# Optimization experiments

Measured on AMD Instinct MI355X. Metric: run time of the kernel, lower is better.

The kernel has to match this reference:

```python
import jax, jax.numpy as jnp
import numpy as np

B, C, T = 128, 19, 1000

def _conv2d(x, w, pad, groups=1):
    return jax.lax.conv_general_dilated(x, w, (1, 1), [(pad[0], pad[0]), (pad[1], pad[1])],
                                        dimension_numbers=('NCHW', 'OIHW', 'NCHW'),
                                        feature_group_count=groups)

def _conv1d(x, w, pad):
    return jax.lax.conv_general_dilated(x, w, (1,), [(pad, pad)],
                                        dimension_numbers=('NCH', 'OIH', 'NCH'))

def _bn(x, g, b, axis=1):
    # eval-mode BatchNorm with running_mean=0, running_var=1 -> pure affine
    shp = [1] * x.ndim
    shp[axis] = -1
    return x * g.reshape(shp) + b.reshape(shp)

def _gat(x, W, a_src, a_dst, bias, src, dst, ew):
    # GATConv, concat=False (head mean); messages scaled by external edge weight ew
    N = x.shape[0]
    H, D = a_src.shape
    h = (x @ W).reshape(N, H, D)
    e = jax.nn.leaky_relu((h * a_src).sum(-1)[src] + (h * a_dst).sum(-1)[dst], 0.2)  # [E,H]
    emax = jax.ops.segment_max(e, dst, num_segments=N)
    ee = jnp.exp(e - emax[dst])
    alpha = ee / (jax.ops.segment_sum(ee, dst, num_segments=N)[dst] + 1e-16)
    msg = (alpha * ew[:, None])[:, :, None] * h[src]  # [E,H,D]
    return jax.ops.segment_sum(msg, dst, num_segments=N).mean(1) + bias

def setup_inputs():
    key = jax.random.key(0)
    ks = iter(jax.random.split(key, 48))
    def nrm(shape, s=0.1):
        return jax.random.normal(next(ks), shape, jnp.float32) * s
    ii = np.arange(C)
    base = np.arange(B)[:, None] * C
    src = (base + np.repeat(ii, C)[None, :]).reshape(-1)
    dst = (base + np.tile(ii, C)[None, :]).reshape(-1)
    return {
        'x': nrm((B, C, T), 1.0),
        'conv1_w': nrm((16, 1, 1, 25)),
        'bn1_g': 1.0 + nrm((16,)), 'bn1_b': nrm((16,)),
        'depth_w': nrm((16, 1, C, 1)),
        'bn2_g': 1.0 + nrm((16,)), 'bn2_b': nrm((16,)),
        'se_w1': nrm((16, 4)), 'se_w2': nrm((4, 16)),
        'sep_w': nrm((16, 16, 1, 16)),
        'bn3_g': 1.0 + nrm((16,)), 'bn3_b': nrm((16,)),
        'ms_w0': nrm((16, 1, 15)), 'ms_g0': 1.0 + nrm((16,)), 'ms_b0': nrm((16,)),
        'ms_w1': nrm((16, 1, 25)), 'ms_g1': 1.0 + nrm((16,)), 'ms_b1': nrm((16,)),
        'ms_w2': nrm((16, 1, 35)), 'ms_g2': 1.0 + nrm((16,)), 'ms_b2': nrm((16,)),
        'adj_w': nrm((32, 1)), 'adj_b': nrm((1,)),
        'gat1_w': nrm((32, 8 * 64), 0.05), 'gat1_as': nrm((8, 64)), 'gat1_ad': nrm((8, 64)), 'gat1_bias': nrm((64,)),
        'skip1_w': nrm((32, 64)), 'skip1_b': nrm((64,)),
        'bng1_g': 1.0 + nrm((64,)), 'bng1_b': nrm((64,)),
        'gat2_w': nrm((64, 8 * 64), 0.05), 'gat2_as': nrm((8, 64)), 'gat2_ad': nrm((8, 64)), 'gat2_bias': nrm((64,)),
        'bng2_g': 1.0 + nrm((64,)), 'bng2_b': nrm((64,)),
        'cls_w1': nrm((64, 64)), 'cls_b1': nrm((64,)),
        'cls_w2': nrm((64, 2)), 'cls_b2': nrm((2,)),
        'edge_index': jnp.asarray(np.stack([src, dst]), dtype=jnp.int32),
        'batch_idx': jnp.repeat(jnp.arange(B, dtype=jnp.int32), C),
    }

def reference(x, conv1_w, bn1_g, bn1_b, depth_w, bn2_g, bn2_b, se_w1, se_w2, sep_w, bn3_g, bn3_b,
              ms_w0, ms_g0, ms_b0, ms_w1, ms_g1, ms_b1, ms_w2, ms_g2, ms_b2,
              adj_w, adj_b, gat1_w, gat1_as, gat1_ad, gat1_bias, skip1_w, skip1_b, bng1_g, bng1_b,
              gat2_w, gat2_as, gat2_ad, gat2_bias, bng2_g, bng2_b, cls_w1, cls_b1, cls_w2, cls_b2,
              edge_index, batch_idx):
    Bn, Cn, Tn = x.shape
    gelu = lambda v: jax.nn.gelu(v, approximate=False)
    # --- EEGNet-style frontend ---
    y = _conv2d(x[:, None], conv1_w, (0, 12))                 # [B,16,C,T]
    y = _bn(y, bn1_g, bn1_b)
    y = _conv2d(y, depth_w, (0, 0), groups=16)                # depthwise over channels -> [B,16,1,T]
    y = jax.nn.elu(_bn(y, bn2_g, bn2_b))
    s = y.mean((2, 3))                                        # SE squeeze [B,16]
    s = jax.nn.sigmoid(gelu(s @ se_w1) @ se_w2)
    y = y * s[:, :, None, None]
    y = y.reshape(Bn, 16, 1, Tn // 4, 4).mean(-1)             # AvgPool2d((1,4))
    y = jax.nn.elu(_bn(_conv2d(y, sep_w, (0, 8)), bn3_g, bn3_b))
    yv = y.mean((2, 3))                                       # AdaptiveAvgPool2d((C,1)): 1->C replicates
    y_nodes = jnp.broadcast_to(yv[:, None, :], (Bn, Cn, 16)).reshape(Bn * Cn, 16)
    # --- per-channel multiscale conv1d ---
    z = x.reshape(Bn * Cn, 1, Tn)
    acc = jax.nn.elu(_bn(_conv1d(z, ms_w0, 7), ms_g0, ms_b0))
    acc = acc + jax.nn.elu(_bn(_conv1d(z, ms_w1, 12), ms_g1, ms_b1))
    acc = acc + jax.nn.elu(_bn(_conv1d(z, ms_w2, 17), ms_g2, ms_b2))
    z = (acc / 3.0).mean(-1)                                  # AdaptiveAvgPool1d(1) -> [N,16]
    feat = jnp.concatenate([y_nodes, z], axis=1)              # [N,32]
    # --- edge-weighted GAT stack ---
    scores = jax.nn.sigmoid(feat @ adj_w + adj_b).reshape(-1)
    src, dst = edge_index[0], edge_index[1]
    ew = scores[src] * scores[dst]
    h = _gat(feat, gat1_w, gat1_as, gat1_ad, gat1_bias, src, dst, ew)
    h = gelu(_bn(h, bng1_g, bng1_b) + feat @ skip1_w + skip1_b)
    h2 = _gat(h, gat2_w, gat2_as, gat2_ad, gat2_bias, src, dst, ew)
    h = gelu(_bn(h2, bng2_g, bng2_b) + h2)
    # --- global mean pool + classifier ---
    gs = jax.ops.segment_sum(h, batch_idx, num_segments=Bn)
    cnt = jax.ops.segment_sum(jnp.ones((Bn * Cn, 1), h.dtype), batch_idx, num_segments=Bn)
    g = gs / cnt
    return gelu(g @ cls_w1 + cls_b1) @ cls_w2 + cls_b2
```

## Files before the change

kernel.cpp:

```cpp
#include <hip/hip_runtime.h>
#include <hip/hip_bf16.h>
#include <math.h>

#define BATCH 128
#define NCH 19
#define TLEN 1000
#define NNODES (BATCH * NCH)

__device__ __forceinline__ float eluf(float x) { return x > 0.f ? x : expm1f(x); }
__device__ __forceinline__ float geluf(float x) { return 0.5f * x * (1.f + erff(x * 0.70710678118654752f)); }
__device__ __forceinline__ float sigf(float x) { return 1.f / (1.f + expf(-x)); }
__device__ __forceinline__ float lrelu(float x) { return x > 0.f ? x : 0.2f * x; }

__global__ __launch_bounds__(256) void k_pool(
    const float* __restrict__ x, const float* __restrict__ w1,
    const float* __restrict__ bn1g, const float* __restrict__ bn1b,
    const float* __restrict__ dw, const float* __restrict__ bn2g,
    const float* __restrict__ bn2b, float* __restrict__ y4g,
    float* __restrict__ ssum) {
  int blk = blockIdx.x;
  int b = blk >> 4, f = blk & 15;
  int tid = threadIdx.x;
  __shared__ float xw[1024];
  __shared__ float dws[19], w1s[25];
  __shared__ float redw[4];
  if (tid < 19) dws[tid] = dw[f * 19 + tid];
  else if (tid >= 32 && tid < 57) w1s[tid - 32] = w1[f * 25 + tid - 32];
  __syncthreads();
  const float* xb = x + (size_t)b * NCH * TLEN;
  for (int i = tid; i < 1024; i += 256) {
    int t = i - 12;
    float v = 0.f;
    if (t >= 0 && t < TLEN) {
#pragma unroll
      for (int c = 0; c < 19; c++) v += dws[c] * xb[c * TLEN + t];
    }
    xw[i] = v;
  }
  __syncthreads();
  float g1 = bn1g[f], b1 = bn1b[f];
  float g2 = bn2g[f], b2 = bn2b[f];
  float sumdw = 0.f;
#pragma unroll
  for (int c = 0; c < 19; c++) sumdw += dws[c];
  float scale = g2 * g1, cb = g2 * b1 * sumdw + b2;
  float part = 0.f;
  if (tid < 250) {
    float pool = 0.f;
#pragma unroll
    for (int q = 0; q < 4; q++) {
      int t = 4 * tid + q;
      float acc = 0.f;
#pragma unroll
      for (int k = 0; k < 25; k++) acc += w1s[k] * xw[t + k];
      pool += eluf(scale * acc + cb);
    }
    part = pool;
    y4g[(size_t)(b * 16 + f) * 250 + tid] = pool * 0.25f;
  }
  int lane = tid & 63, wid = tid >> 6;
  for (int off = 32; off > 0; off >>= 1) part += __shfl_down(part, off, 64);
  if (lane == 0) redw[wid] = part;
  __syncthreads();
  if (tid == 0) ssum[b * 16 + f] = redw[0] + redw[1] + redw[2] + redw[3];
}

__global__ __launch_bounds__(256) void k_sep(
    const float* __restrict__ y4g, const float* __restrict__ ssum,
    const float* __restrict__ sew1, const float* __restrict__ sew2,
    const float* __restrict__ sw, const float* __restrict__ g3,
    const float* __restrict__ b3, float* __restrict__ yv) {
  int blk = blockIdx.x;
  int b = blk >> 4, fo = blk & 15;
  int tid = threadIdx.x;
  __shared__ float yloc[16 * 268];
  __shared__ float sws[256];
  __shared__ float s_s[16], se_s[16], u4[4];
  __shared__ float redw[4];
  sws[tid] = sw[fo * 256 + tid];
  if (tid < 16) s_s[tid] = ssum[b * 16 + tid] * (1.f / 1000.f);
  __syncthreads();
  if (tid < 4) {
    float a = 0.f;
#pragma unroll
    for (int ff = 0; ff < 16; ff++) a += s_s[ff] * sew1[ff * 4 + tid];
    u4[tid] = geluf(a);
  }
  __syncthreads();
  if (tid < 16) {
    float a = 0.f;
#pragma unroll
    for (int j = 0; j < 4; j++) a += u4[j] * sew2[j * 16 + tid];
    se_s[tid] = sigf(a);
  }
  __syncthreads();
#pragma unroll
  for (int fi = 0; fi < 16; fi++) {
    float sc = se_s[fi];
    const float* yr = y4g + (size_t)(b * 16 + fi) * 250;
    for (int j = tid; j < 268; j += 256) {
      float v = (j >= 8 && j < 258) ? yr[j - 8] * sc : 0.f;
      yloc[fi * 268 + j] = v;
    }
  }
  __syncthreads();
  float accsum = 0.f;
  if (tid < 251) {
    float acc = 0.f;
#pragma unroll
    for (int fi = 0; fi < 16; fi++) {
      const float* yr = &yloc[fi * 268 + tid];
      const float* wp = &sws[fi * 16];
#pragma unroll
      for (int k = 0; k < 16; k++) acc += yr[k] * wp[k];
    }
    accsum = eluf(g3[fo] * acc + b3[fo]);
  }
  int lane = tid & 63, wid = tid >> 6;
  for (int off = 32; off > 0; off >>= 1)
    accsum += __shfl_down(accsum, off, 64);
  if (lane == 0) redw[wid] = accsum;
  __syncthreads();
  if (tid == 0)
    yv[b * 16 + fo] = (redw[0] + redw[1] + redw[2] + redw[3]) * (1.f / 251.f);
}

#define RP 8
__global__ __launch_bounds__(256) void k_ms(
    const float* __restrict__ x, const float* __restrict__ w0,
    const float* __restrict__ ga0, const float* __restrict__ bb0,
    const float* __restrict__ w1, const float* __restrict__ ga1,
    const float* __restrict__ bb1, const float* __restrict__ w2,
    const float* __restrict__ ga2, const float* __restrict__ bb2,
    const float* __restrict__ yv, float* __restrict__ feat) {
  int n = blockIdx.x, tid = threadIdx.x;
  __shared__ float xr[1034];
  __shared__ float wst[1200];
  __shared__ float red[256];
  for (int i = tid; i < 1034; i += 256) {
    int t = i - 17;
    xr[i] = (t >= 0 && t < TLEN) ? x[(size_t)n * TLEN + t] : 0.f;
  }
  for (int i = tid; i < 240; i += 256) wst[i] = w0[i];
  for (int i = tid; i < 400; i += 256) wst[240 + i] = w1[i];
  for (int i = tid; i < 560; i += 256) wst[640 + i] = w2[i];
  __syncthreads();

  int f = tid & 15, plane = tid >> 4;
  float wa[15], wb[25], wc[35];
#pragma unroll
  for (int k = 0; k < 15; k++) wa[k] = wst[f * 15 + k];
#pragma unroll
  for (int k = 0; k < 25; k++) wb[k] = wst[240 + f * 25 + k];
#pragma unroll
  for (int k = 0; k < 35; k++) wc[k] = wst[640 + f * 35 + k];
  float g0 = ga0[f], c0 = bb0[f];
  float g1 = ga1[f], c1 = bb1[f];
  float g2 = ga2[f], c2 = bb2[f];

  float z = 0.f;
  for (int base = plane * RP; base < TLEN; base += 16 * RP) {
    float xv[34 + RP];
#pragma unroll
    for (int i = 0; i < 34 + RP; i++) xv[i] = xr[base + i];
#pragma unroll
    for (int r = 0; r < RP; r++) {
      float a0 = 0.f, a1 = 0.f, a2 = 0.f;
#pragma unroll
      for (int k = 0; k < 15; k++) a0 += xv[r + 10 + k] * wa[k];
#pragma unroll
      for (int k = 0; k < 25; k++) a1 += xv[r + 5 + k] * wb[k];
#pragma unroll
      for (int k = 0; k < 35; k++) a2 += xv[r + k] * wc[k];
      z += eluf(g0 * a0 + c0) + eluf(g1 * a1 + c1) + eluf(g2 * a2 + c2);
    }
  }
  red[tid] = z;
  __syncthreads();
  for (int s = 128; s >= 16; s >>= 1) {
    if (tid < s) red[tid] += red[tid + s];
    __syncthreads();
  }
  if (tid < 16) {
    feat[(size_t)n * 32 + 16 + tid] = red[tid] * (1.f / 3000.f);
    feat[(size_t)n * 32 + tid] = yv[(n / 19) * 16 + tid];
  }
}

__global__ __launch_bounds__(256) void k_gat1(
    const float* __restrict__ feat, const float* __restrict__ adjw,
    const float* __restrict__ adjb, const float* __restrict__ gw,
    const float* __restrict__ gas, const float* __restrict__ gad,
    const float* __restrict__ gbias, const float* __restrict__ skw,
    const float* __restrict__ skb, const float* __restrict__ bg,
    const float* __restrict__ bb, float* __restrict__ sc_out,
    float* __restrict__ hfeat) {
  int b = blockIdx.x, tid = threadIdx.x;
  __shared__ float fb[19 * 32];
  __shared__ float h1[19 * 512];
  __shared__ float as_s[19 * 8], ad_s[19 * 8], sc_s[19];
  __shared__ float watt[19 * 8 * 19];
  for (int i = tid; i < 19 * 32; i += 256) fb[i] = feat[(size_t)b * 19 * 32 + i];
  __syncthreads();
  for (int idx = tid; idx < 19 * 512; idx += 256) {
    int i = idx >> 9, o = idx & 511;
    const float* fr = &fb[i * 32];
    float a = 0.f;
#pragma unroll
    for (int c = 0; c < 32; c++) a += fr[c] * gw[c * 512 + o];
    h1[idx] = a;
  }
  if (tid < 19) {
    float a = adjb[0];
#pragma unroll
    for (int c = 0; c < 32; c++) a += fb[tid * 32 + c] * adjw[c];
    float s = sigf(a);
    sc_s[tid] = s;
    sc_out[b * 19 + tid] = s;
  }
  __syncthreads();
  if (tid < 152) {
    int i = tid / 8, h = tid & 7;
    float a = 0.f, d2 = 0.f;
#pragma unroll
    for (int d = 0; d < 64; d++) {
      float hv = h1[i * 512 + h * 64 + d];
      a += hv * gas[h * 64 + d];
      d2 += hv * gad[h * 64 + d];
    }
    as_s[tid] = a;
    ad_s[tid] = d2;
  }
  __syncthreads();
  if (tid < 152) {
    int j = tid / 8, h = tid & 7;
    float adj_ = ad_s[j * 8 + h];
    float ev[19], m = -1e30f;
#pragma unroll
    for (int i = 0; i < 19; i++) {
      float e = lrelu(as_s[i * 8 + h] + adj_);
      ev[i] = e;
      m = fmaxf(m, e);
    }
    float den = 0.f;
#pragma unroll
    for (int i = 0; i < 19; i++) {
      ev[i] = expf(ev[i] - m);
      den += ev[i];
    }
    float inv = 1.f / (den + 1e-16f);
    float scj = sc_s[j];
#pragma unroll
    for (int i = 0; i < 19; i++)
      watt[(j * 8 + h) * 19 + i] = ev[i] * inv * sc_s[i] * scj;
  }
  __syncthreads();
  for (int idx = tid; idx < 19 * 64; idx += 256) {
    int j = idx >> 6, d = idx & 63;
    float acc = 0.f;
#pragma unroll
    for (int h = 0; h < 8; h++) {
      const float* wr = &watt[(j * 8 + h) * 19];
      float a = 0.f;
#pragma unroll
      for (int i = 0; i < 19; i++) a += wr[i] * h1[i * 512 + h * 64 + d];
      acc += a;
    }
    float om = acc * 0.125f + gbias[d];
    float v = bg[d] * om + bb[d];
    float sk = skb[d];
    const float* fr = &fb[j * 32];
#pragma unroll
    for (int c = 0; c < 32; c++) sk += fr[c] * skw[c * 64 + d];
    hfeat[(size_t)(b * 19 + j) * 64 + d] = geluf(v + sk);
  }
}

__global__ __launch_bounds__(256) void k_gat2(
    const float* __restrict__ hfeat, const float* __restrict__ sc_ws,
    const float* __restrict__ gw, const float* __restrict__ gas,
    const float* __restrict__ gad, const float* __restrict__ gbias,
    const float* __restrict__ bg, const float* __restrict__ bb,
    const float* __restrict__ cw1, const float* __restrict__ cb1,
    const float* __restrict__ cw2, const float* __restrict__ cb2,
    float* __restrict__ out) {
  int b = blockIdx.x, tid = threadIdx.x;
  __shared__ float hb[19 * 64];
  __shared__ float h2[19 * 512];
  __shared__ float as_s[19 * 8], ad_s[19 * 8], sc_s[19];
  __shared__ float watt[19 * 8 * 19];
  __shared__ float hout[19 * 64];
  __shared__ float gpool[64], u_s[64];
  for (int i = tid; i < 19 * 64; i += 256) hb[i] = hfeat[(size_t)b * 19 * 64 + i];
  if (tid < 19) sc_s[tid] = sc_ws[b * 19 + tid];
  __syncthreads();
  for (int idx = tid; idx < 19 * 512; idx += 256) {
    int i = idx >> 9, o = idx & 511;
    const float* hr = &hb[i * 64];
    float a = 0.f;
#pragma unroll
    for (int c = 0; c < 64; c++) a += hr[c] * gw[c * 512 + o];
    h2[idx] = a;
  }
  __syncthreads();
  if (tid < 152) {
    int i = tid / 8, h = tid & 7;
    float a = 0.f, d2 = 0.f;
#pragma unroll
    for (int d = 0; d < 64; d++) {
      float hv = h2[i * 512 + h * 64 + d];
      a += hv * gas[h * 64 + d];
      d2 += hv * gad[h * 64 + d];
    }
    as_s[tid] = a;
    ad_s[tid] = d2;
  }
  __syncthreads();
  if (tid < 152) {
    int j = tid / 8, h = tid & 7;
    float adj_ = ad_s[j * 8 + h];
    float ev[19], m = -1e30f;
#pragma unroll
    for (int i = 0; i < 19; i++) {
      float e = lrelu(as_s[i * 8 + h] + adj_);
      ev[i] = e;
      m = fmaxf(m, e);
    }
    float den = 0.f;
#pragma unroll
    for (int i = 0; i < 19; i++) {
      ev[i] = expf(ev[i] - m);
      den += ev[i];
    }
    float inv = 1.f / (den + 1e-16f);
    float scj = sc_s[j];
#pragma unroll
    for (int i = 0; i < 19; i++)
      watt[(j * 8 + h) * 19 + i] = ev[i] * inv * sc_s[i] * scj;
  }
  __syncthreads();
  for (int idx = tid; idx < 19 * 64; idx += 256) {
    int j = idx >> 6, d = idx & 63;
    float acc = 0.f;
#pragma unroll
    for (int h = 0; h < 8; h++) {
      const float* wr = &watt[(j * 8 + h) * 19];
      float a = 0.f;
#pragma unroll
      for (int i = 0; i < 19; i++) a += wr[i] * h2[i * 512 + h * 64 + d];
      acc += a;
    }
    float om = acc * 0.125f + gbias[d];
    float v = bg[d] * om + bb[d] + om;
    hout[idx] = geluf(v);
  }
  __syncthreads();
  if (tid < 64) {
    float a = 0.f;
#pragma unroll
    for (int j = 0; j < 19; j++) a += hout[j * 64 + tid];
    gpool[tid] = a * (1.f / 19.f);
  }
  __syncthreads();
  if (tid < 64) {
    float a = cb1[tid];
#pragma unroll
    for (int d = 0; d < 64; d++) a += gpool[d] * cw1[d * 64 + tid];
    u_s[tid] = geluf(a);
  }
  __syncthreads();
  if (tid < 2) {
    float a = cb2[tid];
#pragma unroll
    for (int e = 0; e < 64; e++) a += u_s[e] * cw2[e * 2 + tid];
    out[b * 2 + tid] = a;
  }
}

extern "C" void kernel_launch(void* const* d_in, const int* in_sizes, int n_in,
                              void* d_out, int out_size, void* d_ws,
                              size_t ws_size, hipStream_t stream) {
  (void)in_sizes; (void)n_in; (void)out_size; (void)ws_size;
  const float* x = (const float*)d_in[0];
  const float* conv1_w = (const float*)d_in[1];
  const float* bn1_g = (const float*)d_in[2];
  const float* bn1_b = (const float*)d_in[3];
  const float* depth_w = (const float*)d_in[4];
  const float* bn2_g = (const float*)d_in[5];
  const float* bn2_b = (const float*)d_in[6];
  const float* se_w1 = (const float*)d_in[7];
  const float* se_w2 = (const float*)d_in[8];
  const float* sep_w = (const float*)d_in[9];
  const float* bn3_g = (const float*)d_in[10];
  const float* bn3_b = (const float*)d_in[11];
  const float* ms_w0 = (const float*)d_in[12];
  const float* ms_g0 = (const float*)d_in[13];
  const float* ms_b0 = (const float*)d_in[14];
  const float* ms_w1 = (const float*)d_in[15];
  const float* ms_g1 = (const float*)d_in[16];
  const float* ms_b1 = (const float*)d_in[17];
  const float* ms_w2 = (const float*)d_in[18];
  const float* ms_g2 = (const float*)d_in[19];
  const float* ms_b2 = (const float*)d_in[20];
  const float* adj_w = (const float*)d_in[21];
  const float* adj_b = (const float*)d_in[22];
  const float* gat1_w = (const float*)d_in[23];
  const float* gat1_as = (const float*)d_in[24];
  const float* gat1_ad = (const float*)d_in[25];
  const float* gat1_bias = (const float*)d_in[26];
  const float* skip1_w = (const float*)d_in[27];
  const float* skip1_b = (const float*)d_in[28];
  const float* bng1_g = (const float*)d_in[29];
  const float* bng1_b = (const float*)d_in[30];
  const float* gat2_w = (const float*)d_in[31];
  const float* gat2_as = (const float*)d_in[32];
  const float* gat2_ad = (const float*)d_in[33];
  const float* gat2_bias = (const float*)d_in[34];
  const float* bng2_g = (const float*)d_in[35];
  const float* bng2_b = (const float*)d_in[36];
  const float* cls_w1 = (const float*)d_in[37];
  const float* cls_b1 = (const float*)d_in[38];
  const float* cls_w2 = (const float*)d_in[39];
  const float* cls_b2 = (const float*)d_in[40];

  float* ws = (float*)d_ws;
  float* yv = ws;
  float* feat = ws + 2048;
  float* scw = ws + 79872;
  float* hfeat = ws + 82304;
  float* y4g = ws + 237952;
  float* ssum = ws + 749952;

  hipLaunchKernelGGL(k_pool, dim3(BATCH * 16), dim3(256), 0, stream,
                     x, conv1_w, bn1_g, bn1_b, depth_w, bn2_g, bn2_b, y4g, ssum);
  hipLaunchKernelGGL(k_sep, dim3(BATCH * 16), dim3(256), 0, stream,
                     y4g, ssum, se_w1, se_w2, sep_w, bn3_g, bn3_b, yv);
  hipLaunchKernelGGL(k_ms, dim3(NNODES), dim3(256), 0, stream,
                     x, ms_w0, ms_g0, ms_b0, ms_w1, ms_g1, ms_b1, ms_w2,
                     ms_g2, ms_b2, yv, feat);
  hipLaunchKernelGGL(k_gat1, dim3(BATCH), dim3(256), 0, stream,
                     feat, adj_w, adj_b, gat1_w, gat1_as, gat1_ad, gat1_bias,
                     skip1_w, skip1_b, bng1_g, bng1_b, scw, hfeat);
  hipLaunchKernelGGL(k_gat2, dim3(BATCH), dim3(256), 0, stream,
                     hfeat, scw, gat2_w, gat2_as, gat2_ad, gat2_bias, bng2_g,
                     bng2_b, cls_w1, cls_b1, cls_w2, cls_b2, (float*)d_out);
}
```

Before: 381.1 us.

## Fuse GAT layers into one kernel, split multiscale conv loops, use fast exp

Merges the two GAT kernels into a single per-batch kernel, so the intermediate hidden features and edge scores stay in shared memory instead of going through global memory, and one launch is dropped. The GAT projection matmuls now keep weight columns in registers per thread and reuse them across all 19 nodes. The multiscale conv loop is split into three separate passes, one per kernel width, to cut peak register pressure. expm1f/expf are replaced with __expf, trading a little accuracy for cheaper transcendentals.

```diff
diff --git a/kernel.cpp b/kernel.cpp
--- a/kernel.cpp
+++ b/kernel.cpp
@@ -7,9 +7,9 @@
 #define TLEN 1000
 #define NNODES (BATCH * NCH)
 
-__device__ __forceinline__ float eluf(float x) { return x > 0.f ? x : expm1f(x); }
+__device__ __forceinline__ float eluf(float x) { return x > 0.f ? x : __expf(x) - 1.f; }
 __device__ __forceinline__ float geluf(float x) { return 0.5f * x * (1.f + erff(x * 0.70710678118654752f)); }
-__device__ __forceinline__ float sigf(float x) { return 1.f / (1.f + expf(-x)); }
+__device__ __forceinline__ float sigf(float x) { return 1.f / (1.f + __expf(-x)); }
 __device__ __forceinline__ float lrelu(float x) { return x > 0.f ? x : 0.2f * x; }
 
 __global__ __launch_bounds__(256) void k_pool(
@@ -147,34 +147,63 @@
   __syncthreads();
 
   int f = tid & 15, plane = tid >> 4;
-  float wa[15], wb[25], wc[35];
-#pragma unroll
-  for (int k = 0; k < 15; k++) wa[k] = wst[f * 15 + k];
-#pragma unroll
-  for (int k = 0; k < 25; k++) wb[k] = wst[240 + f * 25 + k];
-#pragma unroll
-  for (int k = 0; k < 35; k++) wc[k] = wst[640 + f * 35 + k];
-  float g0 = ga0[f], c0 = bb0[f];
-  float g1 = ga1[f], c1 = bb1[f];
-  float g2 = ga2[f], c2 = bb2[f];
-
   float z = 0.f;
-  for (int base = plane * RP; base < TLEN; base += 16 * RP) {
-    float xv[34 + RP];
-#pragma unroll
-    for (int i = 0; i < 34 + RP; i++) xv[i] = xr[base + i];
-#pragma unroll
-    for (int r = 0; r < RP; r++) {
-      float a0 = 0.f, a1 = 0.f, a2 = 0.f;
-#pragma unroll
-      for (int k = 0; k < 15; k++) a0 += xv[r + 10 + k] * wa[k];
-#pragma unroll
-      for (int k = 0; k < 25; k++) a1 += xv[r + 5 + k] * wb[k];
-#pragma unroll
-      for (int k = 0; k < 35; k++) a2 += xv[r + k] * wc[k];
-      z += eluf(g0 * a0 + c0) + eluf(g1 * a1 + c1) + eluf(g2 * a2 + c2);
-    }
-  }
+
+  {
+    float w[15];
+#pragma unroll
+    for (int k = 0; k < 15; k++) w[k] = wst[f * 15 + k];
+    float g = ga0[f], c = bb0[f];
+    for (int base = plane * RP; base < TLEN; base += 16 * RP) {
+      float xv[14 + RP];
+#pragma unroll
+      for (int i = 0; i < 14 + RP; i++) xv[i] = xr[base + 10 + i];
+#pragma unroll
+      for (int r = 0; r < RP; r++) {
+        float a = 0.f;
+#pragma unroll
+        for (int k = 0; k < 15; k++) a += xv[r + k] * w[k];
+        z += eluf(g * a + c);
+      }
+    }
+  }
+  {
+    float w[25];
+#pragma unroll
+    for (int k = 0; k < 25; k++) w[k] = wst[240 + f * 25 + k];
+    float g = ga1[f], c = bb1[f];
+    for (int base = plane * RP; base < TLEN; base += 16 * RP) {
+      float xv[24 + RP];
+#pragma unroll
+      for (int i = 0; i < 24 + RP; i++) xv[i] = xr[base + 5 + i];
+#pragma unroll
+      for (int r = 0; r < RP; r++) {
+        float a = 0.f;
+#pragma unroll
+        for (int k = 0; k < 25; k++) a += xv[r + k] * w[k];
+        z += eluf(g * a + c);
+      }
+    }
+  }
+  {
+    float w[35];
+#pragma unroll
+    for (int k = 0; k < 35; k++) w[k] = wst[640 + f * 35 + k];
+    float g = ga2[f], c = bb2[f];
+    for (int base = plane * RP; base < TLEN; base += 16 * RP) {
+      float xv[34 + RP];
+#pragma unroll
+      for (int i = 0; i < 34 + RP; i++) xv[i] = xr[base + i];
+#pragma unroll
+      for (int r = 0; r < RP; r++) {
+        float a = 0.f;
+#pragma unroll
+        for (int k = 0; k < 35; k++) a += xv[r + k] * w[k];
+        z += eluf(g * a + c);
+      }
+    }
+  }
+
   red[tid] = z;
   __syncthreads();
   for (int s = 128; s >= 16; s >>= 1) {
@@ -187,46 +216,67 @@
   }
 }
 
-__global__ __launch_bounds__(256) void k_gat1(
+__global__ __launch_bounds__(256) void k_gat(
     const float* __restrict__ feat, const float* __restrict__ adjw,
-    const float* __restrict__ adjb, const float* __restrict__ gw,
-    const float* __restrict__ gas, const float* __restrict__ gad,
-    const float* __restrict__ gbias, const float* __restrict__ skw,
-    const float* __restrict__ skb, const float* __restrict__ bg,
-    const float* __restrict__ bb, float* __restrict__ sc_out,
-    float* __restrict__ hfeat) {
+    const float* __restrict__ adjb, const float* __restrict__ g1w,
+    const float* __restrict__ g1as, const float* __restrict__ g1ad,
+    const float* __restrict__ g1bias, const float* __restrict__ skw,
+    const float* __restrict__ skb, const float* __restrict__ bg1,
+    const float* __restrict__ bb1, const float* __restrict__ g2w,
+    const float* __restrict__ g2as, const float* __restrict__ g2ad,
+    const float* __restrict__ g2bias, const float* __restrict__ bg2,
+    const float* __restrict__ bb2, const float* __restrict__ cw1,
+    const float* __restrict__ cb1, const float* __restrict__ cw2,
+    const float* __restrict__ cb2, float* __restrict__ out) {
   int b = blockIdx.x, tid = threadIdx.x;
   __shared__ float fb[19 * 32];
   __shared__ float h1[19 * 512];
   __shared__ float as_s[19 * 8], ad_s[19 * 8], sc_s[19];
   __shared__ float watt[19 * 8 * 19];
+  __shared__ float hb[19 * 64];
+  __shared__ float hout[19 * 64];
+  __shared__ float gpool[64], u_s[64];
+
   for (int i = tid; i < 19 * 32; i += 256) fb[i] = feat[(size_t)b * 19 * 32 + i];
   __syncthreads();
-  for (int idx = tid; idx < 19 * 512; idx += 256) {
-    int i = idx >> 9, o = idx & 511;
-    const float* fr = &fb[i * 32];
-    float a = 0.f;
-#pragma unroll
-    for (int c = 0; c < 32; c++) a += fr[c] * gw[c * 512 + o];
-    h1[idx] = a;
+
+  {
+    float wc0[32], wc1[32];
+#pragma unroll
+    for (int c = 0; c < 32; c++) {
+      wc0[c] = g1w[c * 512 + tid];
+      wc1[c] = g1w[c * 512 + tid + 256];
+    }
+    for (int i = 0; i < 19; i++) {
+      float frow[32];
+#pragma unroll
+      for (int c = 0; c < 32; c++) frow[c] = fb[i * 32 + c];
+      float a0 = 0.f, a1 = 0.f;
+#pragma unroll
+      for (int c = 0; c < 32; c++) {
+        a0 += frow[c] * wc0[c];
+        a1 += frow[c] * wc1[c];
+      }
+      h1[i * 512 + tid] = a0;
+      h1[i * 512 + tid + 256] = a1;
+    }
   }
   if (tid < 19) {
     float a = adjb[0];
 #pragma unroll
     for (int c = 0; c < 32; c++) a += fb[tid * 32 + c] * adjw[c];
-    float s = sigf(a);
-    sc_s[tid] = s;
-    sc_out[b * 19 + tid] = s;
-  }
-  __syncthreads();
+    sc_s[tid] = sigf(a);
+  }
+  __syncthreads();
+
   if (tid < 152) {
     int i = tid / 8, h = tid & 7;
     float a = 0.f, d2 = 0.f;
 #pragma unroll
     for (int d = 0; d < 64; d++) {
       float hv = h1[i * 512 + h * 64 + d];
-      a += hv * gas[h * 64 + d];
-      d2 += hv * gad[h * 64 + d];
+      a += hv * g1as[h * 64 + d];
+      d2 += hv * g1ad[h * 64 + d];
     }
     as_s[tid] = a;
     ad_s[tid] = d2;
@@ -245,7 +295,7 @@
     float den = 0.f;
 #pragma unroll
     for (int i = 0; i < 19; i++) {
-      ev[i] = expf(ev[i] - m);
+      ev[i] = __expf(ev[i] - m);
       den += ev[i];
     }
     float inv = 1.f / (den + 1e-16f);
@@ -266,51 +316,39 @@
       for (int i = 0; i < 19; i++) a += wr[i] * h1[i * 512 + h * 64 + d];
       acc += a;
     }
-    float om = acc * 0.125f + gbias[d];
-    float v = bg[d] * om + bb[d];
+    float om = acc * 0.125f + g1bias[d];
+    float v = bg1[d] * om + bb1[d];
     float sk = skb[d];
     const float* fr = &fb[j * 32];
 #pragma unroll
     for (int c = 0; c < 32; c++) sk += fr[c] * skw[c * 64 + d];
-    hfeat[(size_t)(b * 19 + j) * 64 + d] = geluf(v + sk);
-  }
-}
-
-__global__ __launch_bounds__(256) void k_gat2(
-    const float* __restrict__ hfeat, const float* __restrict__ sc_ws,
-    const float* __restrict__ gw, const float* __restrict__ gas,
-    const float* __restrict__ gad, const float* __restrict__ gbias,
-    const float* __restrict__ bg, const float* __restrict__ bb,
-    const float* __restrict__ cw1, const float* __restrict__ cb1,
-    const float* __restrict__ cw2, const float* __restrict__ cb2,
-    float* __restrict__ out) {
-  int b = blockIdx.x, tid = threadIdx.x;
-  __shared__ float hb[19 * 64];
-  __shared__ float h2[19 * 512];
-  __shared__ float as_s[19 * 8], ad_s[19 * 8], sc_s[19];
-  __shared__ float watt[19 * 8 * 19];
-  __shared__ float hout[19 * 64];
-  __shared__ float gpool[64], u_s[64];
-  for (int i = tid; i < 19 * 64; i += 256) hb[i] = hfeat[(size_t)b * 19 * 64 + i];
-  if (tid < 19) sc_s[tid] = sc_ws[b * 19 + tid];
-  __syncthreads();
-  for (int idx = tid; idx < 19 * 512; idx += 256) {
-    int i = idx >> 9, o = idx & 511;
-    const float* hr = &hb[i * 64];
-    float a = 0.f;
-#pragma unroll
-    for (int c = 0; c < 64; c++) a += hr[c] * gw[c * 512 + o];
-    h2[idx] = a;
-  }
-  __syncthreads();
+    hb[idx] = geluf(v + sk);
+  }
+  __syncthreads();
+
+#pragma unroll
+  for (int oo = 0; oo < 2; oo++) {
+    int o = tid + oo * 256;
+    float wc[64];
+#pragma unroll
+    for (int c = 0; c < 64; c++) wc[c] = g2w[c * 512 + o];
+    for (int i = 0; i < 19; i++) {
+      float a = 0.f;
+#pragma unroll
+      for (int c = 0; c < 64; c++) a += hb[i * 64 + c] * wc[c];
+      h1[i * 512 + o] = a;
+    }
+  }
+  __syncthreads();
+
   if (tid < 152) {
     int i = tid / 8, h = tid & 7;
     float a = 0.f, d2 = 0.f;
 #pragma unroll
     for (int d = 0; d < 64; d++) {
-      float hv = h2[i * 512 + h * 64 + d];
-      a += hv * gas[h * 64 + d];
-      d2 += hv * gad[h * 64 + d];
+      float hv = h1[i * 512 + h * 64 + d];
+      a += hv * g2as[h * 64 + d];
+      d2 += hv * g2ad[h * 64 + d];
     }
     as_s[tid] = a;
     ad_s[tid] = d2;
@@ -329,7 +367,7 @@
     float den = 0.f;
 #pragma unroll
     for (int i = 0; i < 19; i++) {
-      ev[i] = expf(ev[i] - m);
+      ev[i] = __expf(ev[i] - m);
       den += ev[i];
     }
     float inv = 1.f / (den + 1e-16f);
@@ -347,14 +385,15 @@
       const float* wr = &watt[(j * 8 + h) * 19];
       float a = 0.f;
 #pragma unroll
-      for (int i = 0; i < 19; i++) a += wr[i] * h2[i * 512 + h * 64 + d];
+      for (int i = 0; i < 19; i++) a += wr[i] * h1[i * 512 + h * 64 + d];
       acc += a;
     }
-    float om = acc * 0.125f + gbias[d];
-    float v = bg[d] * om + bb[d] + om;
+    float om = acc * 0.125f + g2bias[d];
+    float v = bg2[d] * om + bb2[d] + om;
     hout[idx] = geluf(v);
   }
   __syncthreads();
+
   if (tid < 64) {
     float a = 0.f;
 #pragma unroll
@@ -426,10 +465,8 @@
   float* ws = (float*)d_ws;
   float* yv = ws;
   float* feat = ws + 2048;
-  float* scw = ws + 79872;
-  float* hfeat = ws + 82304;
-  float* y4g = ws + 237952;
-  float* ssum = ws + 749952;
+  float* y4g = ws + 79872;
+  float* ssum = ws + 591872;
 
   hipLaunchKernelGGL(k_pool, dim3(BATCH * 16), dim3(256), 0, stream,
                      x, conv1_w, bn1_g, bn1_b, depth_w, bn2_g, bn2_b, y4g, ssum);
@@ -438,10 +475,9 @@
   hipLaunchKernelGGL(k_ms, dim3(NNODES), dim3(256), 0, stream,
                      x, ms_w0, ms_g0, ms_b0, ms_w1, ms_g1, ms_b1, ms_w2,
                      ms_g2, ms_b2, yv, feat);
-  hipLaunchKernelGGL(k_gat1, dim3(BATCH), dim3(256), 0, stream,
+  hipLaunchKernelGGL(k_gat, dim3(BATCH), dim3(256), 0, stream,
                      feat, adj_w, adj_b, gat1_w, gat1_as, gat1_ad, gat1_bias,
-                     skip1_w, skip1_b, bng1_g, bng1_b, scw, hfeat);
-  hipLaunchKernelGGL(k_gat2, dim3(BATCH), dim3(256), 0, stream,
-                     hfeat, scw, gat2_w, gat2_as, gat2_ad, gat2_bias, bng2_g,
-                     bng2_b, cls_w1, cls_b1, cls_w2, cls_b2, (float*)d_out);
+                     skip1_w, skip1_b, bng1_g, bng1_b, gat2_w, gat2_as,
+                     gat2_ad, gat2_bias, bng2_g, bng2_b, cls_w1, cls_b1,
+                     cls_w2, cls_b2, (float*)d_out);
 }
```

Result: faster. 354.0 us (-7.1%).
